# Kernel tuning notes

Measured on AMD Instinct MI355X. Metric: run time of the kernel, lower is better.

The kernel has to match this reference:

```python
import jax, jax.numpy as jnp
import numpy as np

C0 = 1.0  # speed of sound (units absorbed; distances pre-scaled)
FS = 1.0  # sampling frequency

A, E, S = 4, 128, 3072   # n_angles, n_elements, n_samples
NZ, NX = 512, 256        # image grid


def setup_inputs() -> dict:
    key = jax.random.key(0)
    k1, k2, k3, k4 = jax.random.split(key, 4)
    scale = (S / 2.0) - 1.0  # spread delays over the valid sample range
    d_tx = jax.random.uniform(k1, (A, NZ, NX), dtype=jnp.float32) * scale
    d_rx = jax.random.uniform(k2, (E, NZ, NX), dtype=jnp.float32) * scale
    apod = jax.random.uniform(k3, (E, NZ, NX), dtype=jnp.float32)
    rf = jax.random.normal(k4, (A, E, S), dtype=jnp.float32)
    t0 = jnp.zeros((A,), dtype=jnp.float32)
    return {"d_tx": d_tx, "d_rx": d_rx, "apod": apod, "rf": rf, "t0": t0}


def reference(d_tx, d_rx, apod, rf, t0):
    a, e, s = rf.shape
    nz, nx = d_tx.shape[1], d_tx.shape[2]
    # total delay in samples: [A, E, nz, nx]
    delays = ((d_tx[:, None] + d_rx[None]) / C0 - t0[:, None, None, None]) * FS
    x0 = jnp.floor(delays)
    w = delays - x0                      # linear interp weight
    i0 = x0.astype(jnp.int32)
    i1 = i0 + 1

    def gather(idx):
        # rf: [A, E, S]; idx: [A, E, nz, nx] -> gathered [A, E, nz, nx]
        g = jnp.take_along_axis(rf, jnp.clip(idx, 0, s - 1).reshape(a, e, -1), axis=2)
        return g.reshape(a, e, nz, nx)

    # grid_sample(padding_mode='zeros', align_corners=True): out-of-range taps contribute 0
    v0 = jnp.where((i0 >= 0) & (i0 <= s - 1), gather(i0), 0.0)
    v1 = jnp.where((i1 >= 0) & (i1 <= s - 1), gather(i1), 0.0)
    sampled = v0 * (1.0 - w) + v1 * w    # [A, E, nz, nx]
    # apodization-weighted sum over elements -> [A, nz, nx]
    das = jnp.einsum('aezx,ezx->azx', sampled, apod)
    return das
```

## Files before the change

### kernel.cpp

```cpp
#include <hip/hip_runtime.h>


#define A_N 4
#define E_N 128
#define S_N 3072
#define NPIX_N (512 * 256)
#define TPB 512
#define PXT 8
#define TILE (TPB * PXT)
#define TILES (NPIX_N / TILE)
#define ESPLIT 16
#define EPB (E_N / ESPLIT)
#define STAGE_ITERS ((A_N * S_N / 4) / TPB)

__global__ __launch_bounds__(TPB, 2) void das_kernel(
    const float* __restrict__ d_tx, const float* __restrict__ d_rx,
    const float* __restrict__ apod, const float* __restrict__ rf,
    const float* __restrict__ t0,  float* __restrict__ out)
{
    __shared__ float lds_rf[A_N * S_N];
    const int tid = threadIdx.x;
    const int px0 = blockIdx.x * TILE + tid;
    const int e0  = blockIdx.y * EPB;

    int sbase[STAGE_ITERS];
#pragma unroll
    for (int j = 0; j < STAGE_ITERS; ++j) {
        int idx = tid + j * TPB;
        int a   = idx / (S_N / 4);
        int s4  = idx - a * (S_N / 4);
        sbase[j] = a * (E_N * S_N) + s4 * 4;
    }

    float acc[A_N][PXT];
    float dta[A_N][PXT];
#pragma unroll
    for (int a = 0; a < A_N; ++a) {
        const float t0a = t0[a];
#pragma unroll
        for (int k = 0; k < PXT; ++k) {
            dta[a][k] = d_tx[a * NPIX_N + px0 + k * TPB] - t0a;
            acc[a][k] = 0.0f;
        }
    }

    for (int ei = 0; ei < EPB; ++ei) {
        const int e = e0 + ei;
        __syncthreads();
#pragma unroll
        for (int j = 0; j < STAGE_ITERS; ++j) {
            float4 v = *(const float4*)(rf + sbase[j] + e * S_N);
            ((float4*)lds_rf)[tid + j * TPB] = v;
        }
        __syncthreads();

        const float* __restrict__ drx_row = d_rx + (size_t)e * NPIX_N;
        const float* __restrict__ ap_row  = apod + (size_t)e * NPIX_N;
#pragma unroll
        for (int k = 0; k < PXT; ++k) {
            const int p = px0 + k * TPB;
            const float drx = drx_row[p];
            const float ap  = ap_row[p];
#pragma unroll
            for (int a = 0; a < A_N; ++a) {
                float delay = dta[a][k] + drx;
                float x0 = floorf(delay);
                float w  = delay - x0;
                int i0 = (int)x0;
                i0 = min(max(i0, 0), S_N - 2);
                float v0 = lds_rf[a * S_N + i0];
                float v1 = lds_rf[a * S_N + i0 + 1];
                acc[a][k] += (v0 + w * (v1 - v0)) * ap;
            }
        }
    }

#pragma unroll
    for (int a = 0; a < A_N; ++a)
#pragma unroll
        for (int k = 0; k < PXT; ++k)
            atomicAdd(&out[a * NPIX_N + px0 + k * TPB], acc[a][k]);
}

extern "C" void kernel_launch(void* const* d_in, const int* in_sizes, int n_in,
                              void* d_out, int out_size, void* d_ws, size_t ws_size,
                              hipStream_t stream) {
    const float* d_tx = (const float*)d_in[0];
    const float* d_rx = (const float*)d_in[1];
    const float* apod = (const float*)d_in[2];
    const float* rf   = (const float*)d_in[3];
    const float* t0   = (const float*)d_in[4];
    float* out = (float*)d_out;

    hipMemsetAsync(out, 0, (size_t)out_size * sizeof(float), stream);
    dim3 grid(TILES, ESPLIT);
    das_kernel<<<grid, TPB, 0, stream>>>(d_tx, d_rx, apod, rf, t0, out);
}
```

Measured before the change: 203.9 us.

## Double-buffer RF staging with async global-to-LDS loads and halve element split

RF rows for the next element are now loaded directly into a second LDS buffer with `global_load_lds` while the current element's pixels are interpolated. This replaces the synchronous load-store staging and its two barriers per element with one barrier per iteration. ESPLIT drops from 16 to 8, so each block covers more elements and the output needs half as many atomic adds. The cost is 96KB of LDS per block, which likely allows only one resident block per CU and leaves fewer waves to hide d_rx/apod global-load latency.

```diff
diff --git a/kernel.cpp b/kernel.cpp
--- a/kernel.cpp
+++ b/kernel.cpp
@@ -9,28 +9,44 @@
 #define PXT 8
 #define TILE (TPB * PXT)
 #define TILES (NPIX_N / TILE)
-#define ESPLIT 16
+#define ESPLIT 8
 #define EPB (E_N / ESPLIT)
-#define STAGE_ITERS ((A_N * S_N / 4) / TPB)
+#define CPA (S_N / 256)
+#define CHUNKS (A_N * CPA)
+#define WAVES (TPB / 64)
+#define CPW (CHUNKS / WAVES)
+
+__device__ __forceinline__ void ld_lds16(const float* g, float* l) {
+    __builtin_amdgcn_global_load_lds(
+        (const __attribute__((address_space(1))) void*)g,
+        (__attribute__((address_space(3))) void*)l, 16, 0, 0);
+}
 
 __global__ __launch_bounds__(TPB, 2) void das_kernel(
     const float* __restrict__ d_tx, const float* __restrict__ d_rx,
     const float* __restrict__ apod, const float* __restrict__ rf,
     const float* __restrict__ t0,  float* __restrict__ out)
 {
-    __shared__ float lds_rf[A_N * S_N];
-    const int tid = threadIdx.x;
-    const int px0 = blockIdx.x * TILE + tid;
-    const int e0  = blockIdx.y * EPB;
+    __shared__ float lds_rf[2][A_N * S_N];
+    const int tid  = threadIdx.x;
+    const int wid  = tid >> 6;
+    const int lane = tid & 63;
+    const int px0  = blockIdx.x * TILE + tid;
+    const int e0   = blockIdx.y * EPB;
 
-    int sbase[STAGE_ITERS];
+    auto stage = [&](int b, int e) {
 #pragma unroll
-    for (int j = 0; j < STAGE_ITERS; ++j) {
-        int idx = tid + j * TPB;
-        int a   = idx / (S_N / 4);
-        int s4  = idx - a * (S_N / 4);
-        sbase[j] = a * (E_N * S_N) + s4 * 4;
-    }
+        for (int j = 0; j < CPW; ++j) {
+            const int chunk = wid * CPW + j;
+            const int a = chunk / CPA;
+            const int c = chunk - a * CPA;
+            const float* g = rf + ((size_t)(a * E_N + e)) * S_N + c * 256 + lane * 4;
+            float* l = &lds_rf[b][a * S_N + c * 256];
+            ld_lds16(g, l);
+        }
+    };
+
+    stage(0, e0);
 
     float acc[A_N][PXT];
     float dta[A_N][PXT];
@@ -44,18 +60,18 @@
         }
     }
 
+    __syncthreads();
+
     for (int ei = 0; ei < EPB; ++ei) {
-        const int e = e0 + ei;
-        __syncthreads();
-#pragma unroll
-        for (int j = 0; j < STAGE_ITERS; ++j) {
-            float4 v = *(const float4*)(rf + sbase[j] + e * S_N);
-            ((float4*)lds_rf)[tid + j * TPB] = v;
-        }
-        __syncthreads();
+        const int e   = e0 + ei;
+        const int cur = ei & 1;
+
+        if (ei + 1 < EPB) stage(cur ^ 1, e + 1);
 
         const float* __restrict__ drx_row = d_rx + (size_t)e * NPIX_N;
         const float* __restrict__ ap_row  = apod + (size_t)e * NPIX_N;
+        const float* __restrict__ L = lds_rf[cur];
+
 #pragma unroll
         for (int k = 0; k < PXT; ++k) {
             const int p = px0 + k * TPB;
@@ -68,11 +84,13 @@
                 float w  = delay - x0;
                 int i0 = (int)x0;
                 i0 = min(max(i0, 0), S_N - 2);
-                float v0 = lds_rf[a * S_N + i0];
-                float v1 = lds_rf[a * S_N + i0 + 1];
+                float v0 = L[a * S_N + i0];
+                float v1 = L[a * S_N + i0 + 1];
                 acc[a][k] += (v0 + w * (v1 - v0)) * ap;
             }
         }
+
+        __syncthreads();
     }
 
 #pragma unroll
```

Result: faster. 194.0 us (-4.9%).
